# Kernel optimization log

Hardware: AMD Instinct MI355X
Metric: run time of the kernel (lower is better)

## Reference

```python
import jax, jax.numpy as jnp
import numpy as np

N = 32768; D = 384; P = 3; CORR_D = 2 * 49 * P * P  # 882
G_KK = 4096; G_JK = 512
EPS = 1e-3  # LayerNorm eps in the torch module

FLOAT_NAMES = ("net","inp","corr","corr_w1","corr_b1","corr_w2","corr_b2","corr_ln_g","corr_ln_b","corr_w3","corr_b3","norm_g","norm_b","c1_w1","c1_b1","c1_w2","c1_b2","c2_w1","c2_b1","c2_w2","c2_b2","kk_fw","kk_fb","kk_gw","kk_gb","kk_hw","kk_hb","ij_fw","ij_fb","ij_gw","ij_gb","ij_hw","ij_hb","g_ln1_g","g_ln1_b","g1_gw","g1_gb","g1_r1w","g1_r1b","g1_r2w","g1_r2b","g_ln2_g","g_ln2_b","g2_gw","g2_gb","g2_r1w","g2_r1b","g2_r2w","g2_r2b","d_w","d_b","w_w","w_b")

def _ln(x, g, b):
    m = jnp.mean(x, -1, keepdims=True)
    v = jnp.mean((x - m) ** 2, -1, keepdims=True)
    return (x - m) * jax.lax.rsqrt(v + EPS) * g + b

def _mlp2(x, w1, b1, w2, b2):
    return jax.nn.relu(x @ w1 + b1) @ w2 + b2

def _gated_residual(x, gw, gb, r1w, r1b, r2w, r2b):
    gate = jax.nn.sigmoid(x @ gw + gb)
    res = jax.nn.relu(x @ r1w + r1b) @ r2w + r2b
    return x + gate * res

def _soft_agg(x, jx, fw, fb, gw, gb, hw, hb, num_groups):
    # x: [N, D]; jx: [N] group ids -> group-wise softmax weighted sum
    logits = x @ gw + gb
    feats = x @ fw + fb
    gmax = jax.ops.segment_max(logits, jx, num_segments=num_groups)
    e = jnp.exp(logits - gmax[jx])
    den = jax.ops.segment_sum(e, jx, num_segments=num_groups)
    w = e / (den[jx] + 1e-12)
    y = jax.ops.segment_sum(feats * w, jx, num_segments=num_groups)
    return (y @ hw + hb)[jx]

def _forward(p, nix, njx, ukk, ujk):
    # corr encoder MLP
    h = jax.nn.relu(p["corr"] @ p["corr_w1"] + p["corr_b1"]) @ p["corr_w2"] + p["corr_b2"]
    h = jax.nn.relu(_ln(h, p["corr_ln_g"], p["corr_ln_b"])) @ p["corr_w3"] + p["corr_b3"]
    net = p["net"] + p["inp"] + h
    net = _ln(net, p["norm_g"], p["norm_b"])
    mask_ix = (nix >= 0).astype(net.dtype).reshape(1, -1, 1)
    mask_jx = (njx >= 0).astype(net.dtype).reshape(1, -1, 1)
    net = net + _mlp2(mask_ix * net[:, nix], p["c1_w1"], p["c1_b1"], p["c1_w2"], p["c1_b2"])
    net = net + _mlp2(mask_jx * net[:, njx], p["c2_w1"], p["c2_b1"], p["c2_w2"], p["c2_b2"])
    net = net + _soft_agg(net[0], ukk, p["kk_fw"], p["kk_fb"], p["kk_gw"], p["kk_gb"], p["kk_hw"], p["kk_hb"], G_KK)[None]
    net = net + _soft_agg(net[0], ujk, p["ij_fw"], p["ij_fb"], p["ij_gw"], p["ij_gb"], p["ij_hw"], p["ij_hb"], G_JK)[None]
    net = _ln(net, p["g_ln1_g"], p["g_ln1_b"])
    net = _gated_residual(net, p["g1_gw"], p["g1_gb"], p["g1_r1w"], p["g1_r1b"], p["g1_r2w"], p["g1_r2b"])
    net = _ln(net, p["g_ln2_g"], p["g_ln2_b"])
    net = _gated_residual(net, p["g2_gw"], p["g2_gb"], p["g2_r1w"], p["g2_r1b"], p["g2_r2w"], p["g2_r2b"])
    r = jax.nn.relu(net)
    d = r @ p["d_w"] + p["d_b"]               # GradClip is identity in forward
    w = jax.nn.sigmoid(r @ p["w_w"] + p["w_b"])
    return net, d, w

def setup_inputs() -> dict:
    key = jax.random.key(0)
    it = iter(jax.random.split(key, 64))
    def pr(*shape):
        return jax.random.normal(next(it), shape, dtype=jnp.float32) * 0.02
    z = lambda *s: jnp.zeros(s, jnp.float32)
    o = lambda *s: jnp.ones(s, jnp.float32)
    inp = {
        "net": jax.random.normal(next(it), (1, N, D), dtype=jnp.float32),
        "inp": jax.random.normal(next(it), (1, N, D), dtype=jnp.float32),
        "corr": jax.random.normal(next(it), (1, N, CORR_D), dtype=jnp.float32),
        "nix": jax.random.randint(next(it), (N,), 0, N),
        "njx": jax.random.randint(next(it), (N,), 0, N),
        "ukk": jax.random.randint(next(it), (N,), 0, G_KK),
        "ujk": jax.random.randint(next(it), (N,), 0, G_JK),
        "corr_w1": pr(CORR_D, D), "corr_b1": z(D), "corr_w2": pr(D, D), "corr_b2": z(D),
        "corr_ln_g": o(D), "corr_ln_b": z(D), "corr_w3": pr(D, D), "corr_b3": z(D),
        "norm_g": o(D), "norm_b": z(D),
        "c1_w1": pr(D, D), "c1_b1": z(D), "c1_w2": pr(D, D), "c1_b2": z(D),
        "c2_w1": pr(D, D), "c2_b1": z(D), "c2_w2": pr(D, D), "c2_b2": z(D),
        "kk_fw": pr(D, D), "kk_fb": z(D), "kk_gw": pr(D, D), "kk_gb": z(D), "kk_hw": pr(D, D), "kk_hb": z(D),
        "ij_fw": pr(D, D), "ij_fb": z(D), "ij_gw": pr(D, D), "ij_gb": z(D), "ij_hw": pr(D, D), "ij_hb": z(D),
        "g_ln1_g": o(D), "g_ln1_b": z(D),
        "g1_gw": pr(D, D), "g1_gb": z(D), "g1_r1w": pr(D, D), "g1_r1b": z(D), "g1_r2w": pr(D, D), "g1_r2b": z(D),
        "g_ln2_g": o(D), "g_ln2_b": z(D),
        "g2_gw": pr(D, D), "g2_gb": z(D), "g2_r1w": pr(D, D), "g2_r1b": z(D), "g2_r2w": pr(D, D), "g2_r2b": z(D),
        "d_w": pr(D, 2), "d_b": z(2), "w_w": pr(D, 2), "w_b": z(2),
    }
    return inp

def reference(net, inp, corr, corr_w1, corr_b1, corr_w2, corr_b2, corr_ln_g, corr_ln_b, corr_w3, corr_b3, norm_g, norm_b, c1_w1, c1_b1, c1_w2, c1_b2, c2_w1, c2_b1, c2_w2, c2_b2, kk_fw, kk_fb, kk_gw, kk_gb, kk_hw, kk_hb, ij_fw, ij_fb, ij_gw, ij_gb, ij_hw, ij_hb, g_ln1_g, g_ln1_b, g1_gw, g1_gb, g1_r1w, g1_r1b, g1_r2w, g1_r2b, g_ln2_g, g_ln2_b, g2_gw, g2_gb, g2_r1w, g2_r1b, g2_r2w, g2_r2b, d_w, d_b, w_w, w_b, nix, njx, ukk, ujk):
    loc = locals()
    fl = {k: loc[k] for k in FLOAT_NAMES}
    return _forward(fl, nix, njx, ukk, ujk)
```

## Files before the change

### kernel.cpp

```cpp
#include <hip/hip_runtime.h>
#include <hip/hip_bf16.h>
#include <math.h>

#define NR 32768
#define DD 384
#define CDM 882
#define CDMP 896

typedef float f4 __attribute__((ext_vector_type(4)));
typedef float f32x4 __attribute__((ext_vector_type(4)));
typedef __bf16 bf16x8 __attribute__((ext_vector_type(8)));
typedef __bf16 bf16x4 __attribute__((ext_vector_type(4)));

__device__ inline f4 ld4(const float* p) { f4 v; __builtin_memcpy(&v, p, 16); return v; }
__device__ inline void st4(float* p, f4 v) { __builtin_memcpy(p, &v, 16); }
__device__ inline bf16x8 ld8h(const __bf16* p) { bf16x8 v; __builtin_memcpy(&v, p, 16); return v; }
__device__ inline void st8h(__bf16* p, bf16x8 v) { __builtin_memcpy(p, &v, 16); }

__device__ inline void gl_lds16(const void* g, void* l) {
  __builtin_amdgcn_global_load_lds(
      (const __attribute__((address_space(1))) void*)g,
      (__attribute__((address_space(3))) void*)l, 16, 0, 0);
}

__device__ inline float gred16(float v) {
#pragma unroll
  for (int o = 1; o < 16; o <<= 1) v += __shfl_xor(v, o, 64);
  return v;
}

__global__ __launch_bounds__(256) void corr2bf16_k(const float* __restrict__ src,
                                                   __bf16* __restrict__ dst) {
  int i = blockIdx.x * 256 + threadIdx.x;
  int row = i / 112, c8 = (i - row * 112) * 8;
  const float* sp = src + (size_t)row * CDM + c8;
  bf16x8 h;
  if (c8 + 8 <= CDM) {
#pragma unroll
    for (int e = 0; e < 8; ++e) h[e] = (__bf16)sp[e];
  } else {
#pragma unroll
    for (int e = 0; e < 8; ++e) h[e] = (c8 + e < CDM) ? (__bf16)sp[e] : (__bf16)0.f;
  }
  st8h(dst + (size_t)row * CDMP + c8, h);
}

struct WPtrs { const float* w[18]; };

__global__ __launch_bounds__(256) void trans_all_k(WPtrs P, __bf16* __restrict__ dst) {
  int wi = blockIdx.y;
  const float* W = P.w[wi];
  __bf16* WT = dst + (size_t)wi * DD * DD;
  int i = blockIdx.x * 256 + threadIdx.x;
  if (i >= DD * DD) return;
  int n = i / DD, k = i - n * DD;
  WT[i] = (__bf16)W[(size_t)k * DD + n];
}

__global__ __launch_bounds__(256) void trans_corr_k(const float* __restrict__ W,
                                                    __bf16* __restrict__ WT) {
  int i = blockIdx.x * 256 + threadIdx.x;
  if (i >= DD * CDMP) return;
  int n = i / CDMP, k = i - n * CDMP;
  WT[i] = (k < CDM) ? (__bf16)W[(size_t)k * DD + n] : (__bf16)0.f;
}

template <int EPI, int AFP32>
__global__ __launch_bounds__(512, 1) void gemm_k(
    const void* __restrict__ Av, const __bf16* __restrict__ WT,
    const float* __restrict__ bias, __bf16* __restrict__ OUT,
    const __bf16* __restrict__ XRES, const int* __restrict__ idx,
    const __bf16* __restrict__ zpage, int M, int K) {
  __shared__ __align__(16) __bf16 sm[2 * 32768];
  const int t = threadIdx.x;
  const int w = t >> 6, lane = t & 63;
  const int m0 = blockIdx.x * 128;
  const int fr = lane & 15, fq = lane >> 4;
  const int wr = (w >> 2) * 64, wc = (w & 3) * 96;

  const __bf16* aptr[2];
  int aadv[2];
  const __bf16* bptr[6];
#pragma unroll
  for (int j = 0; j < 2; ++j) {
    int rloc = w * 16 + j * 8 + (lane >> 3);
    int cch = (lane & 7) ^ (rloc & 7);
    if constexpr (!AFP32) {
      int ar = idx ? idx[m0 + rloc] : (m0 + rloc);
      if (ar >= 0) { aptr[j] = (const __bf16*)Av + (size_t)ar * K + cch * 8; aadv[j] = 64; }
      else { aptr[j] = zpage; aadv[j] = 0; }
    }
  }
#pragma unroll
  for (int j = 0; j < 6; ++j) {
    int rloc = w * 48 + j * 8 + (lane >> 3);
    int cch = (lane & 7) ^ (rloc & 7);
    bptr[j] = WT + (size_t)rloc * K + cch * 8;
  }
  const float* Af = (const float*)Av;
  const int NT = K >> 6;

  f32x4 acc[4][6];
#pragma unroll
  for (int a = 0; a < 4; ++a)
#pragma unroll
    for (int b = 0; b < 6; ++b)
#pragma unroll
      for (int j = 0; j < 4; ++j) acc[a][b][j] = 0.f;

  auto stageG = [&](int buf) {
    __bf16* As = sm + buf * 32768;
    __bf16* Bs = As + 8192;
#pragma unroll
    for (int j = 0; j < 2; ++j) {
      gl_lds16(aptr[j], &As[(w * 16 + j * 8) * 64]);
      aptr[j] += aadv[j];
    }
#pragma unroll
    for (int j = 0; j < 6; ++j) {
      gl_lds16(bptr[j], &Bs[(w * 48 + j * 8) * 64]);
      bptr[j] += 64;
    }
  };

  auto stageF = [&](int k0) {
    __bf16* As = sm;
    __bf16* Bs = sm + 8192;
#pragma unroll
    for (int j = 0; j < 2; ++j) {
      int rr = (t >> 3) + 64 * j;
      int cc = t & 7;
      const float* ap = Af + (size_t)(m0 + rr) * K + k0 + cc * 8;
      f4 v0 = ld4(ap), v1 = ld4(ap + 4);
      bf16x8 h;
#pragma unroll
      for (int e = 0; e < 4; ++e) { h[e] = (__bf16)v0[e]; h[4 + e] = (__bf16)v1[e]; }
      *reinterpret_cast<bf16x8*>(&As[rr * 64 + ((cc ^ (rr & 7)) << 3)]) = h;
    }
#pragma unroll
    for (int j = 0; j < 6; ++j) {
      gl_lds16(bptr[j], &Bs[(w * 48 + j * 8) * 64]);
      bptr[j] += 64;
    }
  };

  auto compute = [&](int buf) {
    const __bf16* As = sm + buf * 32768;
    const __bf16* Bs = As + 8192;
#pragma unroll
    for (int kk2 = 0; kk2 < 2; ++kk2) {
      bf16x8 af[4];
      bf16x8 bv[6];
#pragma unroll
      for (int mi = 0; mi < 4; ++mi) {
        int rr = wr + mi * 16 + fr;
        af[mi] = *reinterpret_cast<const bf16x8*>(
            &As[rr * 64 + (((fq + kk2 * 4) ^ (rr & 7)) << 3)]);
      }
#pragma unroll
      for (int ni = 0; ni < 6; ++ni) {
        int rr = wc + ni * 16 + fr;
        bv[ni] = *reinterpret_cast<const bf16x8*>(
            &Bs[rr * 64 + (((fq + kk2 * 4) ^ (rr & 7)) << 3)]);
      }
#pragma unroll
      for (int mi = 0; mi < 4; ++mi)
#pragma unroll
        for (int ni = 0; ni < 6; ++ni)
          acc[mi][ni] = __builtin_amdgcn_mfma_f32_16x16x32_bf16(af[mi], bv[ni],
                                                                acc[mi][ni], 0, 0, 0);
    }
  };

  if constexpr (AFP32) {
    for (int tt = 0; tt < NT; ++tt) {
      if (tt) __syncthreads();
      stageF(tt << 6);
      __syncthreads();
      compute(0);
    }
  } else {
    stageG(0);
    int buf = 0;
    for (int tt = 0; tt < NT; ++tt) {
      if (tt + 1 < NT) {
        stageG(buf ^ 1);
        asm volatile("s_waitcnt vmcnt(8)" ::: "memory");
      } else {
        asm volatile("s_waitcnt vmcnt(0)" ::: "memory");
      }
      __builtin_amdgcn_s_barrier();
      __builtin_amdgcn_sched_barrier(0);
      compute(buf);
      __builtin_amdgcn_s_barrier();
      __builtin_amdgcn_sched_barrier(0);
      buf ^= 1;
    }
  }

#pragma unroll
  for (int mi = 0; mi < 4; ++mi)
#pragma unroll
    for (int ni = 0; ni < 6; ++ni) {
      int col = wc + ni * 16 + fr;
      float bvv = bias[col];
#pragma unroll
      for (int j = 0; j < 4; ++j) {
        int row = m0 + wr + mi * 16 + fq * 4 + j;
        size_t o = (size_t)row * DD + col;
        float v = acc[mi][ni][j] + bvv;
        if constexpr (EPI == 0) {
          OUT[o] = (__bf16)v;
        } else if constexpr (EPI == 1) {
          OUT[o] = (__bf16)fmaxf(v, 0.f);
        } else if constexpr (EPI == 2) {
          OUT[o] = (__bf16)((float)OUT[o] + v);
        } else {
          float gl = (float)OUT[o];
          float g = 1.f / (1.f + expf(-gl));
          OUT[o] = (__bf16)((float)XRES[o] + g * v);
        }
      }
    }
}

template <int RELU>
__global__ __launch_bounds__(256) void ln_k(const __bf16* __restrict__ x,
                                            const float* __restrict__ g,
                                            const float* __restrict__ b,
                                            __bf16* __restrict__ out) {
  int w = threadIdx.x >> 6, lane = threadIdx.x & 63;
  int s = lane & 15, qq = lane >> 4;
  int row = blockIdx.x * 16 + w * 4 + qq;
  size_t base = (size_t)row * DD;
  float v[24];
#pragma unroll
  for (int i = 0; i < 3; ++i) {
    bf16x8 h = ld8h(x + base + (s + 16 * i) * 8);
#pragma unroll
    for (int e = 0; e < 8; ++e) v[i * 8 + e] = (float)h[e];
  }
  float sm = 0.f;
#pragma unroll
  for (int i = 0; i < 24; ++i) sm += v[i];
  sm = gred16(sm);
  float mean = sm * (1.f / 384.f);
  float qs = 0.f;
#pragma unroll
  for (int i = 0; i < 24; ++i) { float d = v[i] - mean; qs += d * d; }
  qs = gred16(qs);
  float rs = rsqrtf(qs * (1.f / 384.f) + 1e-3f);
#pragma unroll
  for (int i = 0; i < 3; ++i) {
    int col = (s + 16 * i) * 8;
    f4 g0 = ld4(g + col), g1 = ld4(g + col + 4);
    f4 b0 = ld4(b + col), b1 = ld4(b + col + 4);
    bf16x8 o;
#pragma unroll
    for (int e = 0; e < 4; ++e) {
      float y0 = (v[i * 8 + e] - mean) * rs * g0[e] + b0[e];
      float y1 = (v[i * 8 + 4 + e] - mean) * rs * g1[e] + b1[e];
      if (RELU) { y0 = fmaxf(y0, 0.f); y1 = fmaxf(y1, 0.f); }
      o[e] = (__bf16)y0; o[4 + e] = (__bf16)y1;
    }
    st8h(out + base + col, o);
  }
}

__global__ __launch_bounds__(256) void ln3_k(const float* __restrict__ x1,
                                             const float* __restrict__ x2,
                                             const __bf16* __restrict__ x3,
                                             const float* __restrict__ g,
                                             const float* __restrict__ b,
                                             __bf16* __restrict__ out) {
  int w = threadIdx.x >> 6, lane = threadIdx.x & 63;
  int s = lane & 15, qq = lane >> 4;
  int row = blockIdx.x * 16 + w * 4 + qq;
  size_t base = (size_t)row * DD;
  float v[24];
#pragma unroll
  for (int i = 0; i < 3; ++i) {
    int col = (s + 16 * i) * 8;
    f4 a0 = ld4(x1 + base + col), a1 = ld4(x1 + base + col + 4);
    f4 c0 = ld4(x2 + base + col), c1 = ld4(x2 + base + col + 4);
    bf16x8 h = ld8h(x3 + base + col);
#pragma unroll
    for (int e = 0; e < 4; ++e) {
      v[i * 8 + e] = a0[e] + c0[e] + (float)h[e];
      v[i * 8 + 4 + e] = a1[e] + c1[e] + (float)h[4 + e];
    }
  }
  float sm = 0.f;
#pragma unroll
  for (int i = 0; i < 24; ++i) sm += v[i];
  sm = gred16(sm);
  float mean = sm * (1.f / 384.f);
  float qs = 0.f;
#pragma unroll
  for (int i = 0; i < 24; ++i) { float d = v[i] - mean; qs += d * d; }
  qs = gred16(qs);
  float rs = rsqrtf(qs * (1.f / 384.f) + 1e-3f);
#pragma unroll
  for (int i = 0; i < 3; ++i) {
    int col = (s + 16 * i) * 8;
    f4 g0 = ld4(g + col), g1 = ld4(g + col + 4);
    f4 b0 = ld4(b + col), b1 = ld4(b + col + 4);
    bf16x8 o;
#pragma unroll
    for (int e = 0; e < 4; ++e) {
      o[e] = (__bf16)((v[i * 8 + e] - mean) * rs * g0[e] + b0[e]);
      o[4 + e] = (__bf16)((v[i * 8 + 4 + e] - mean) * rs * g1[e] + b1[e]);
    }
    st8h(out + base + col, o);
  }
}

__global__ __launch_bounds__(256) void hist_k(const int* __restrict__ gid,
                                              int* __restrict__ cnt, int n) {
  int i = blockIdx.x * 256 + threadIdx.x;
  if (i < n) atomicAdd(&cnt[gid[i]], 1);
}

__global__ __launch_bounds__(256) void scan_k(const int* __restrict__ cnt,
                                              int* __restrict__ off,
                                              int* __restrict__ curb, int G) {
  __shared__ int ls[256];
  int t = threadIdx.x;
  int per = G / 256;
  int base = t * per;
  int s = 0;
  for (int i = 0; i < per; ++i) s += cnt[base + i];
  ls[t] = s;
  __syncthreads();
  for (int o = 1; o < 256; o <<= 1) {
    int v = (t >= o) ? ls[t - o] : 0;
    __syncthreads();
    ls[t] += v;
    __syncthreads();
  }
  int run = (t == 0) ? 0 : ls[t - 1];
  for (int i = 0; i < per; ++i) {
    off[base + i] = run;
    run += cnt[base + i];
    curb[base + i] = 0;
  }
  if (t == 255) off[G] = run;
}

__global__ __launch_bounds__(256) void scatter_k(const int* __restrict__ gid,
                                                 const int* __restrict__ off,
                                                 int* __restrict__ cur,
                                                 int* __restrict__ rows, int n) {
  int i = blockIdx.x * 256 + threadIdx.x;
  if (i >= n) return;
  int g = gid[i];
  int p = atomicAdd(&cur[g], 1);
  rows[off[g] + p] = i;
}

__global__ __launch_bounds__(384) void segagg_k(const __bf16* __restrict__ L,
                                                const __bf16* __restrict__ Ft,
                                                const int* __restrict__ rows,
                                                const int* __restrict__ off,
                                                float* __restrict__ yb) {
  int g = blockIdx.x;
  int c = threadIdx.x;
  int s = off[g], e = off[g + 1];
  float mx = -3.0e38f;
  for (int p = s; p < e; ++p) {
    int r = rows[p];
    mx = fmaxf(mx, (float)L[(size_t)r * DD + c]);
  }
  float num = 0.f, den = 0.f;
  for (int p = s; p < e; ++p) {
    int r = rows[p];
    float lv = (float)L[(size_t)r * DD + c];
    float fv = (float)Ft[(size_t)r * DD + c];
    float ev = expf(lv - mx);
    den += ev;
    num += fv * ev;
  }
  yb[(size_t)g * DD + c] = num / (den + 1e-12f);
}

__global__ __launch_bounds__(256) void addgather_k(__bf16* __restrict__ X,
                                                   const __bf16* __restrict__ z,
                                                   const int* __restrict__ gid) {
  int i = blockIdx.x * 256 + threadIdx.x;
  int row = i / 48, c = (i - row * 48) * 8;
  int g = gid[row];
  size_t lo = (size_t)row * DD + c;
  bf16x8 a = ld8h(X + lo);
  bf16x8 zz = ld8h(z + (size_t)g * DD + c);
  bf16x8 o;
#pragma unroll
  for (int e = 0; e < 8; ++e) o[e] = (__bf16)((float)a[e] + (float)zz[e]);
  st8h(X + lo, o);
}

__global__ __launch_bounds__(256) void final_k(const __bf16* __restrict__ net,
                                               const float* __restrict__ dw,
                                               const float* __restrict__ db,
                                               const float* __restrict__ ww,
                                               const float* __restrict__ wb,
                                               float* __restrict__ out) {
  int w = threadIdx.x >> 6, lane = threadIdx.x & 63;
  int s = lane & 15, qq = lane >> 4;
  int row = blockIdx.x * 16 + w * 4 + qq;
  size_t base = (size_t)row * DD;
  float d0 = 0, d1 = 0, w0 = 0, w1 = 0;
#pragma unroll
  for (int i = 0; i < 3; ++i) {
    int col = (s + 16 * i) * 8;
    bf16x8 h = ld8h(net + base + col);
    f4 o0, o1;
#pragma unroll
    for (int e = 0; e < 4; ++e) {
      float x0 = (float)h[e], x1 = (float)h[4 + e];
      o0[e] = x0; o1[e] = x1;
      float r0 = fmaxf(x0, 0.f), r1 = fmaxf(x1, 0.f);
      int c0 = col + e, c1 = col + 4 + e;
      d0 += r0 * dw[2 * c0] + r1 * dw[2 * c1];
      d1 += r0 * dw[2 * c0 + 1] + r1 * dw[2 * c1 + 1];
      w0 += r0 * ww[2 * c0] + r1 * ww[2 * c1];
      w1 += r0 * ww[2 * c0 + 1] + r1 * ww[2 * c1 + 1];
    }
    st4(out + base + col, o0);
    st4(out + base + col + 4, o1);
  }
  d0 = gred16(d0); d1 = gred16(d1); w0 = gred16(w0); w1 = gred16(w1);
  if (s == 0) {
    float* outd = out + (size_t)NR * DD;
    float* outw = outd + (size_t)NR * 2;
    outd[2 * row] = d0 + db[0];
    outd[2 * row + 1] = d1 + db[1];
    outw[2 * row] = 1.f / (1.f + expf(-(w0 + wb[0])));
    outw[2 * row + 1] = 1.f / (1.f + expf(-(w1 + wb[1])));
  }
}

extern "C" void kernel_launch(void* const* d_in, const int* in_sizes, int n_in,
                              void* d_out, int out_size, void* d_ws, size_t ws_size,
                              hipStream_t stream) {
  const float* in_net = (const float*)d_in[0];
  const float* in_inp = (const float*)d_in[1];
  const float* in_corr = (const float*)d_in[2];
  const int* nix = (const int*)d_in[3];
  const int* njx = (const int*)d_in[4];
  const int* ukk = (const int*)d_in[5];
  const int* ujk = (const int*)d_in[6];
  auto F = [&](int i) { return (const float*)d_in[i]; };

  constexpr size_t MiB = 1024 * 1024;
  constexpr size_t SZ_ACT = (size_t)NR * DD * 2;
  char* ws = (char*)d_ws;
  __bf16* Xc = (__bf16*)(ws);
  __bf16* T2b = (__bf16*)(ws);
  __bf16* Fb = (__bf16*)(ws + SZ_ACT);
  __bf16* zb = (__bf16*)(ws + 2 * SZ_ACT);
  float* yb = (float*)(ws + 2 * SZ_ACT + 3 * MiB);
  __bf16* T1b = (__bf16*)(ws + 60 * MiB);
  char* p = ws + 84 * MiB;
  int* rows = (int*)p; p += (size_t)NR * 4;
  int* off = (int*)p; p += 32768;
  int* cnt = (int*)p; p += 16384;
  int* curb = (int*)p; p += 16384;
  __bf16* wt_all = (__bf16*)p; p += (size_t)18 * DD * DD * 2;
  __bf16* wt_corr1 = (__bf16*)p; p += (size_t)DD * CDMP * 2;
  __bf16* zpage = (__bf16*)p;

  const int widx[18] = {17, 19, 21, 23, 25, 27, 29, 31, 33, 35, 39, 41, 43, 47, 49, 51, 9, 13};
  WPtrs P;
  for (int i = 0; i < 18; ++i) P.w[i] = F(widx[i]);
  auto WTp = [&](int i) { return wt_all + (size_t)i * DD * DD; };

  hipMemsetAsync(zpage, 0, 256, stream);
  trans_all_k<<<dim3(576, 18), 256, 0, stream>>>(P, wt_all);
  trans_corr_k<<<1344, 256, 0, stream>>>(F(7), wt_corr1);
  corr2bf16_k<<<NR * 112 / 256, 256, 0, stream>>>(in_corr, Xc);

  auto GEMM = [&](int epi, int afp32, const void* A, const __bf16* WT, const float* bias,
                  __bf16* OUT, const __bf16* XRES, const int* idx, int M, int K) {
    dim3 g(M / 128), b(512);
    if (afp32) {
      gemm_k<0, 1><<<g, b, 0, stream>>>(A, WT, bias, OUT, XRES, idx, zpage, M, K);
    } else {
      switch (epi) {
        case 0: gemm_k<0, 0><<<g, b, 0, stream>>>(A, WT, bias, OUT, XRES, idx, zpage, M, K); break;
        case 1: gemm_k<1, 0><<<g, b, 0, stream>>>(A, WT, bias, OUT, XRES, idx, zpage, M, K); break;
        case 2: gemm_k<2, 0><<<g, b, 0, stream>>>(A, WT, bias, OUT, XRES, idx, zpage, M, K); break;
        default: gemm_k<3, 0><<<g, b, 0, stream>>>(A, WT, bias, OUT, XRES, idx, zpage, M, K); break;
      }
    }
  };

  auto SEGAGG = [&](const int* gid, int G, const __bf16* L, const __bf16* Ft) {
    hipMemsetAsync(cnt, 0, (size_t)G * 4, stream);
    hist_k<<<NR / 256, 256, 0, stream>>>(gid, cnt, NR);
    scan_k<<<1, 256, 0, stream>>>(cnt, off, curb, G);
    scatter_k<<<NR / 256, 256, 0, stream>>>(gid, off, curb, rows, NR);
    segagg_k<<<G, 384, 0, stream>>>(L, Ft, rows, off, yb);
  };

  const int LNG = NR / 16;
  const int SEGB = NR * 48 / 256;

  GEMM(1, 0, Xc, wt_corr1, F(8), T1b, nullptr, nullptr, NR, CDMP);
  GEMM(0, 0, T1b, WTp(16), F(10), T2b, nullptr, nullptr, NR, DD);
  ln_k<1><<<LNG, 256, 0, stream>>>(T2b, F(11), F(12), T1b);
  GEMM(0, 0, T1b, WTp(17), F(14), T2b, nullptr, nullptr, NR, DD);
  ln3_k<<<LNG, 256, 0, stream>>>(in_net, in_inp, T2b, F(15), F(16), T1b);
  GEMM(1, 0, T1b, WTp(0), F(18), T2b, nullptr, nix, NR, DD);
  GEMM(2, 0, T2b, WTp(1), F(20), T1b, nullptr, nullptr, NR, DD);
  GEMM(1, 0, T1b, WTp(2), F(22), T2b, nullptr, njx, NR, DD);
  GEMM(2, 0, T2b, WTp(3), F(24), T1b, nullptr, nullptr, NR, DD);
  GEMM(0, 0, T1b, WTp(5), F(28), T2b, nullptr, nullptr, NR, DD);
  GEMM(0, 0, T1b, WTp(4), F(26), Fb, nullptr, nullptr, NR, DD);
  SEGAGG(ukk, 4096, T2b, Fb);
  GEMM(0, 1, yb, WTp(6), F(30), zb, nullptr, nullptr, 4096, DD);
  addgather_k<<<SEGB, 256, 0, stream>>>(T1b, zb, ukk);
  GEMM(0, 0, T1b, WTp(8), F(34), T2b, nullptr, nullptr, NR, DD);
  GEMM(0, 0, T1b, WTp(7), F(32), Fb, nullptr, nullptr, NR, DD);
  SEGAGG(ujk, 512, T2b, Fb);
  GEMM(0, 1, yb, WTp(9), F(36), zb, nullptr, nullptr, 512, DD);
  addgather_k<<<SEGB, 256, 0, stream>>>(T1b, zb, ujk);
  ln_k<0><<<LNG, 256, 0, stream>>>(T1b, F(37), F(38), T2b);
  GEMM(0, 0, T2b, WTp(10), F(40), Fb, nullptr, nullptr, NR, DD);
  GEMM(1, 0, T2b, WTp(11), F(42), T1b, nullptr, nullptr, NR, DD);
  GEMM(3, 0, T1b, WTp(12), F(44), Fb, T2b, nullptr, NR, DD);
  ln_k<0><<<LNG, 256, 0, stream>>>(Fb, F(45), F(46), T1b);
  GEMM(0, 0, T1b, WTp(13), F(48), T2b, nullptr, nullptr, NR, DD);
  GEMM(1, 0, T1b, WTp(14), F(50), Fb, nullptr, nullptr, NR, DD);
  GEMM(3, 0, Fb, WTp(15), F(52), T2b, T1b, nullptr, NR, DD);
  final_k<<<LNG, 256, 0, stream>>>(T2b, F(53), F(54), F(55), F(56), (float*)d_out);
}
```

Baseline: 666.2 us.

## Fuse LayerNorms and output head into GEMM epilogues; batch segment index build

Row-wise LayerNorm is moved into the GEMM epilogue through new epilogue modes. Each block reduces row sums and sums of squares across the four column warps through LDS, so the standalone ln_k, ln3_k and final_k passes over the activations are no longer needed. The gated-residual GEMMs now apply the following LayerNorm directly, and the last GEMM also writes the fp32 output plus the 2-wide d and w heads. The second add-gather is merged with the next LayerNorm, and the histogram, scan and scatter for both group ids run once up front instead of per aggregation. In exchange, variance is computed as E[x^2]-mean^2 in fp32, which is less numerically robust, and the epilogues use more registers and add extra barriers.

```diff
diff --git a/kernel.cpp b/kernel.cpp
--- a/kernel.cpp
+++ b/kernel.cpp
@@ -65,18 +65,23 @@
   WT[i] = (k < CDM) ? (__bf16)W[(size_t)k * DD + n] : (__bf16)0.f;
 }
 
+struct GP {
+  const void* A; const __bf16* WT; const float* bias; __bf16* OUT;
+  const __bf16* XRES; const __bf16* GIN;
+  const float* p0; const float* p1; const float* p2; const float* p3;
+  float* fout; const float* net32; const float* inp32;
+  const int* idx; const __bf16* zpage; int M; int K;
+};
+
 template <int EPI, int AFP32>
-__global__ __launch_bounds__(512, 1) void gemm_k(
-    const void* __restrict__ Av, const __bf16* __restrict__ WT,
-    const float* __restrict__ bias, __bf16* __restrict__ OUT,
-    const __bf16* __restrict__ XRES, const int* __restrict__ idx,
-    const __bf16* __restrict__ zpage, int M, int K) {
+__global__ __launch_bounds__(512, 1) void gemm_k(GP gp) {
   __shared__ __align__(16) __bf16 sm[2 * 32768];
   const int t = threadIdx.x;
   const int w = t >> 6, lane = t & 63;
   const int m0 = blockIdx.x * 128;
   const int fr = lane & 15, fq = lane >> 4;
   const int wr = (w >> 2) * 64, wc = (w & 3) * 96;
+  const int K = gp.K;
 
   const __bf16* aptr[2];
   int aadv[2];
@@ -86,18 +91,18 @@
     int rloc = w * 16 + j * 8 + (lane >> 3);
     int cch = (lane & 7) ^ (rloc & 7);
     if constexpr (!AFP32) {
-      int ar = idx ? idx[m0 + rloc] : (m0 + rloc);
-      if (ar >= 0) { aptr[j] = (const __bf16*)Av + (size_t)ar * K + cch * 8; aadv[j] = 64; }
-      else { aptr[j] = zpage; aadv[j] = 0; }
+      int ar = gp.idx ? gp.idx[m0 + rloc] : (m0 + rloc);
+      if (ar >= 0) { aptr[j] = (const __bf16*)gp.A + (size_t)ar * K + cch * 8; aadv[j] = 64; }
+      else { aptr[j] = gp.zpage; aadv[j] = 0; }
     }
   }
 #pragma unroll
   for (int j = 0; j < 6; ++j) {
     int rloc = w * 48 + j * 8 + (lane >> 3);
     int cch = (lane & 7) ^ (rloc & 7);
-    bptr[j] = WT + (size_t)rloc * K + cch * 8;
-  }
-  const float* Af = (const float*)Av;
+    bptr[j] = gp.WT + (size_t)rloc * K + cch * 8;
+  }
+  const float* Af = (const float*)gp.A;
   const int NT = K >> 6;
 
   f32x4 acc[4][6];
@@ -198,47 +203,229 @@
     }
   }
 
+  const int nw = w & 3;
+  float bcol[6];
+#pragma unroll
+  for (int ni = 0; ni < 6; ++ni) bcol[ni] = gp.bias[wc + ni * 16 + fr];
 #pragma unroll
   for (int mi = 0; mi < 4; ++mi)
 #pragma unroll
-    for (int ni = 0; ni < 6; ++ni) {
-      int col = wc + ni * 16 + fr;
-      float bvv = bias[col];
-#pragma unroll
-      for (int j = 0; j < 4; ++j) {
-        int row = m0 + wr + mi * 16 + fq * 4 + j;
-        size_t o = (size_t)row * DD + col;
-        float v = acc[mi][ni][j] + bvv;
-        if constexpr (EPI == 0) {
-          OUT[o] = (__bf16)v;
-        } else if constexpr (EPI == 1) {
-          OUT[o] = (__bf16)fmaxf(v, 0.f);
-        } else if constexpr (EPI == 2) {
-          OUT[o] = (__bf16)((float)OUT[o] + v);
-        } else {
-          float gl = (float)OUT[o];
-          float g = 1.f / (1.f + expf(-gl));
-          OUT[o] = (__bf16)((float)XRES[o] + g * v);
+    for (int ni = 0; ni < 6; ++ni)
+#pragma unroll
+      for (int j = 0; j < 4; ++j) acc[mi][ni][j] += bcol[ni];
+
+  if constexpr (EPI <= 2) {
+#pragma unroll
+    for (int mi = 0; mi < 4; ++mi)
+#pragma unroll
+      for (int ni = 0; ni < 6; ++ni) {
+        int col = wc + ni * 16 + fr;
+#pragma unroll
+        for (int j = 0; j < 4; ++j) {
+          int row = m0 + wr + mi * 16 + fq * 4 + j;
+          size_t o = (size_t)row * DD + col;
+          float v = acc[mi][ni][j];
+          if constexpr (EPI == 0) gp.OUT[o] = (__bf16)v;
+          else if constexpr (EPI == 1) gp.OUT[o] = (__bf16)fmaxf(v, 0.f);
+          else gp.OUT[o] = (__bf16)((float)gp.OUT[o] + v);
         }
       }
-    }
-}
-
-template <int RELU>
-__global__ __launch_bounds__(256) void ln_k(const __bf16* __restrict__ x,
-                                            const float* __restrict__ g,
-                                            const float* __restrict__ b,
-                                            __bf16* __restrict__ out) {
+  } else {
+    if constexpr (EPI == 5) {
+#pragma unroll
+      for (int mi = 0; mi < 4; ++mi)
+#pragma unroll
+        for (int ni = 0; ni < 6; ++ni) {
+          int col = wc + ni * 16 + fr;
+#pragma unroll
+          for (int j = 0; j < 4; ++j) {
+            int row = m0 + wr + mi * 16 + fq * 4 + j;
+            size_t o = (size_t)row * DD + col;
+            acc[mi][ni][j] += gp.net32[o] + gp.inp32[o];
+          }
+        }
+    }
+    if constexpr (EPI == 6 || EPI == 7) {
+#pragma unroll
+      for (int mi = 0; mi < 4; ++mi)
+#pragma unroll
+        for (int ni = 0; ni < 6; ++ni) {
+          int col = wc + ni * 16 + fr;
+#pragma unroll
+          for (int j = 0; j < 4; ++j) {
+            int row = m0 + wr + mi * 16 + fq * 4 + j;
+            size_t o = (size_t)row * DD + col;
+            float gl = (float)gp.GIN[o];
+            float sg = 1.f / (1.f + expf(-gl));
+            acc[mi][ni][j] = (float)gp.XRES[o] + sg * acc[mi][ni][j];
+          }
+        }
+    }
+    __syncthreads();
+    if constexpr (EPI != 7) {
+      float s1[4][4], s2[4][4];
+#pragma unroll
+      for (int mi = 0; mi < 4; ++mi)
+#pragma unroll
+        for (int j = 0; j < 4; ++j) { s1[mi][j] = 0.f; s2[mi][j] = 0.f; }
+#pragma unroll
+      for (int mi = 0; mi < 4; ++mi)
+#pragma unroll
+        for (int ni = 0; ni < 6; ++ni)
+#pragma unroll
+          for (int j = 0; j < 4; ++j) {
+            float v = acc[mi][ni][j];
+            s1[mi][j] += v;
+            s2[mi][j] += v * v;
+          }
+#pragma unroll
+      for (int o = 1; o < 16; o <<= 1)
+#pragma unroll
+        for (int mi = 0; mi < 4; ++mi)
+#pragma unroll
+          for (int j = 0; j < 4; ++j) {
+            s1[mi][j] += __shfl_xor(s1[mi][j], o, 64);
+            s2[mi][j] += __shfl_xor(s2[mi][j], o, 64);
+          }
+      float* lsum = (float*)sm;
+      float* lsq = lsum + 512;
+      if (fr == 0) {
+#pragma unroll
+        for (int mi = 0; mi < 4; ++mi)
+#pragma unroll
+          for (int j = 0; j < 4; ++j) {
+            int rr = wr + mi * 16 + fq * 4 + j;
+            lsum[rr * 4 + nw] = s1[mi][j];
+            lsq[rr * 4 + nw] = s2[mi][j];
+          }
+      }
+      __syncthreads();
+      float mn[4][4], rs[4][4];
+#pragma unroll
+      for (int mi = 0; mi < 4; ++mi)
+#pragma unroll
+        for (int j = 0; j < 4; ++j) {
+          int rr = wr + mi * 16 + fq * 4 + j;
+          float S1 = lsum[rr * 4] + lsum[rr * 4 + 1] + lsum[rr * 4 + 2] + lsum[rr * 4 + 3];
+          float S2 = lsq[rr * 4] + lsq[rr * 4 + 1] + lsq[rr * 4 + 2] + lsq[rr * 4 + 3];
+          float m = S1 * (1.f / 384.f);
+          float va = S2 * (1.f / 384.f) - m * m;
+          mn[mi][j] = m;
+          rs[mi][j] = rsqrtf(va + 1e-3f);
+        }
+#pragma unroll
+      for (int ni = 0; ni < 6; ++ni) {
+        int col = wc + ni * 16 + fr;
+        float gg = gp.p0[col], bb = gp.p1[col];
+#pragma unroll
+        for (int mi = 0; mi < 4; ++mi)
+#pragma unroll
+          for (int j = 0; j < 4; ++j) {
+            int row = m0 + wr + mi * 16 + fq * 4 + j;
+            float y = (acc[mi][ni][j] - mn[mi][j]) * rs[mi][j] * gg + bb;
+            if constexpr (EPI == 4) y = fmaxf(y, 0.f);
+            gp.OUT[(size_t)row * DD + col] = (__bf16)y;
+          }
+      }
+    } else {
+      float c0[6], c1[6], c2[6], c3[6];
+#pragma unroll
+      for (int ni = 0; ni < 6; ++ni) {
+        int col = wc + ni * 16 + fr;
+        c0[ni] = gp.p0[2 * col];
+        c1[ni] = gp.p0[2 * col + 1];
+        c2[ni] = gp.p2[2 * col];
+        c3[ni] = gp.p2[2 * col + 1];
+      }
+      float dt[4][4][4];
+#pragma unroll
+      for (int mi = 0; mi < 4; ++mi)
+#pragma unroll
+        for (int j = 0; j < 4; ++j)
+#pragma unroll
+          for (int q = 0; q < 4; ++q) dt[mi][j][q] = 0.f;
+#pragma unroll
+      for (int mi = 0; mi < 4; ++mi)
+#pragma unroll
+        for (int ni = 0; ni < 6; ++ni) {
+          int col = wc + ni * 16 + fr;
+#pragma unroll
+          for (int j = 0; j < 4; ++j) {
+            int row = m0 + wr + mi * 16 + fq * 4 + j;
+            float v = acc[mi][ni][j];
+            gp.fout[(size_t)row * DD + col] = v;
+            float r = fmaxf(v, 0.f);
+            dt[mi][j][0] += r * c0[ni];
+            dt[mi][j][1] += r * c1[ni];
+            dt[mi][j][2] += r * c2[ni];
+            dt[mi][j][3] += r * c3[ni];
+          }
+        }
+#pragma unroll
+      for (int o = 1; o < 16; o <<= 1)
+#pragma unroll
+        for (int mi = 0; mi < 4; ++mi)
+#pragma unroll
+          for (int j = 0; j < 4; ++j)
+#pragma unroll
+            for (int q = 0; q < 4; ++q)
+              dt[mi][j][q] += __shfl_xor(dt[mi][j][q], o, 64);
+      float* lt = (float*)sm;
+      if (fr == 0) {
+#pragma unroll
+        for (int mi = 0; mi < 4; ++mi)
+#pragma unroll
+          for (int j = 0; j < 4; ++j) {
+            int rr = wr + mi * 16 + fq * 4 + j;
+#pragma unroll
+            for (int q = 0; q < 4; ++q) lt[(rr * 4 + nw) * 4 + q] = dt[mi][j][q];
+          }
+      }
+      __syncthreads();
+      if (nw == 0 && fr == 0) {
+        float* fd = gp.fout + (size_t)NR * DD;
+        float* fw = fd + (size_t)NR * 2;
+#pragma unroll
+        for (int mi = 0; mi < 4; ++mi)
+#pragma unroll
+          for (int j = 0; j < 4; ++j) {
+            int rr = wr + mi * 16 + fq * 4 + j;
+            int row = m0 + rr;
+            float T[4];
+#pragma unroll
+            for (int q = 0; q < 4; ++q)
+              T[q] = lt[(rr * 4 + 0) * 4 + q] + lt[(rr * 4 + 1) * 4 + q] +
+                     lt[(rr * 4 + 2) * 4 + q] + lt[(rr * 4 + 3) * 4 + q];
+            fd[2 * row] = T[0] + gp.p1[0];
+            fd[2 * row + 1] = T[1] + gp.p1[1];
+            fw[2 * row] = 1.f / (1.f + expf(-(T[2] + gp.p3[0])));
+            fw[2 * row + 1] = 1.f / (1.f + expf(-(T[3] + gp.p3[1])));
+          }
+      }
+    }
+  }
+}
+
+__global__ __launch_bounds__(256) void ln_ag_k(const __bf16* __restrict__ X,
+                                               const __bf16* __restrict__ z,
+                                               const int* __restrict__ gid,
+                                               const float* __restrict__ g,
+                                               const float* __restrict__ b,
+                                               __bf16* __restrict__ out) {
   int w = threadIdx.x >> 6, lane = threadIdx.x & 63;
   int s = lane & 15, qq = lane >> 4;
   int row = blockIdx.x * 16 + w * 4 + qq;
+  int gr = gid[row];
   size_t base = (size_t)row * DD;
+  size_t zbase = (size_t)gr * DD;
   float v[24];
 #pragma unroll
   for (int i = 0; i < 3; ++i) {
-    bf16x8 h = ld8h(x + base + (s + 16 * i) * 8);
-#pragma unroll
-    for (int e = 0; e < 8; ++e) v[i * 8 + e] = (float)h[e];
+    int col = (s + 16 * i) * 8;
+    bf16x8 h = ld8h(X + base + col);
+    bf16x8 zz = ld8h(z + zbase + col);
+#pragma unroll
+    for (int e = 0; e < 8; ++e) v[i * 8 + e] = (float)h[e] + (float)zz[e];
   }
   float sm = 0.f;
 #pragma unroll
@@ -258,56 +445,6 @@
     bf16x8 o;
 #pragma unroll
     for (int e = 0; e < 4; ++e) {
-      float y0 = (v[i * 8 + e] - mean) * rs * g0[e] + b0[e];
-      float y1 = (v[i * 8 + 4 + e] - mean) * rs * g1[e] + b1[e];
-      if (RELU) { y0 = fmaxf(y0, 0.f); y1 = fmaxf(y1, 0.f); }
-      o[e] = (__bf16)y0; o[4 + e] = (__bf16)y1;
-    }
-    st8h(out + base + col, o);
-  }
-}
-
-__global__ __launch_bounds__(256) void ln3_k(const float* __restrict__ x1,
-                                             const float* __restrict__ x2,
-                                             const __bf16* __restrict__ x3,
-                                             const float* __restrict__ g,
-                                             const float* __restrict__ b,
-                                             __bf16* __restrict__ out) {
-  int w = threadIdx.x >> 6, lane = threadIdx.x & 63;
-  int s = lane & 15, qq = lane >> 4;
-  int row = blockIdx.x * 16 + w * 4 + qq;
-  size_t base = (size_t)row * DD;
-  float v[24];
-#pragma unroll
-  for (int i = 0; i < 3; ++i) {
-    int col = (s + 16 * i) * 8;
-    f4 a0 = ld4(x1 + base + col), a1 = ld4(x1 + base + col + 4);
-    f4 c0 = ld4(x2 + base + col), c1 = ld4(x2 + base + col + 4);
-    bf16x8 h = ld8h(x3 + base + col);
-#pragma unroll
-    for (int e = 0; e < 4; ++e) {
-      v[i * 8 + e] = a0[e] + c0[e] + (float)h[e];
-      v[i * 8 + 4 + e] = a1[e] + c1[e] + (float)h[4 + e];
-    }
-  }
-  float sm = 0.f;
-#pragma unroll
-  for (int i = 0; i < 24; ++i) sm += v[i];
-  sm = gred16(sm);
-  float mean = sm * (1.f / 384.f);
-  float qs = 0.f;
-#pragma unroll
-  for (int i = 0; i < 24; ++i) { float d = v[i] - mean; qs += d * d; }
-  qs = gred16(qs);
-  float rs = rsqrtf(qs * (1.f / 384.f) + 1e-3f);
-#pragma unroll
-  for (int i = 0; i < 3; ++i) {
-    int col = (s + 16 * i) * 8;
-    f4 g0 = ld4(g + col), g1 = ld4(g + col + 4);
-    f4 b0 = ld4(b + col), b1 = ld4(b + col + 4);
-    bf16x8 o;
-#pragma unroll
-    for (int e = 0; e < 4; ++e) {
       o[e] = (__bf16)((v[i * 8 + e] - mean) * rs * g0[e] + b0[e]);
       o[4 + e] = (__bf16)((v[i * 8 + 4 + e] - mean) * rs * g1[e] + b1[e]);
     }
@@ -315,16 +452,16 @@
   }
 }
 
-__global__ __launch_bounds__(256) void hist_k(const int* __restrict__ gid,
-                                              int* __restrict__ cnt, int n) {
+__global__ __launch_bounds__(256) void hist2_k(const int* __restrict__ ukk,
+                                               const int* __restrict__ ujk,
+                                               int* __restrict__ ckk,
+                                               int* __restrict__ cij) {
   int i = blockIdx.x * 256 + threadIdx.x;
-  if (i < n) atomicAdd(&cnt[gid[i]], 1);
-}
-
-__global__ __launch_bounds__(256) void scan_k(const int* __restrict__ cnt,
-                                              int* __restrict__ off,
-                                              int* __restrict__ curb, int G) {
-  __shared__ int ls[256];
+  atomicAdd(&ckk[ukk[i]], 1);
+  atomicAdd(&cij[ujk[i]], 1);
+}
+
+__device__ inline void scan_body(const int* cnt, int* off, int* curb, int G, int* ls) {
   int t = threadIdx.x;
   int per = G / 256;
   int base = t * per;
@@ -347,15 +484,26 @@
   if (t == 255) off[G] = run;
 }
 
-__global__ __launch_bounds__(256) void scatter_k(const int* __restrict__ gid,
-                                                 const int* __restrict__ off,
-                                                 int* __restrict__ cur,
-                                                 int* __restrict__ rows, int n) {
+__global__ __launch_bounds__(256) void scan2_k(const int* ckk, int* okk, int* qkk,
+                                               const int* cij, int* oij, int* qij) {
+  __shared__ int ls[256];
+  if (blockIdx.x == 0) scan_body(ckk, okk, qkk, 4096, ls);
+  else scan_body(cij, oij, qij, 512, ls);
+}
+
+__global__ __launch_bounds__(256) void scatter2_k(const int* __restrict__ ukk,
+                                                  const int* __restrict__ ujk,
+                                                  const int* __restrict__ okk,
+                                                  int* __restrict__ qkk,
+                                                  int* __restrict__ rkk,
+                                                  const int* __restrict__ oij,
+                                                  int* __restrict__ qij,
+                                                  int* __restrict__ rij) {
   int i = blockIdx.x * 256 + threadIdx.x;
-  if (i >= n) return;
-  int g = gid[i];
-  int p = atomicAdd(&cur[g], 1);
-  rows[off[g] + p] = i;
+  int g1 = ukk[i];
+  rkk[okk[g1] + atomicAdd(&qkk[g1], 1)] = i;
+  int g2 = ujk[i];
+  rij[oij[g2] + atomicAdd(&qij[g2], 1)] = i;
 }
 
 __global__ __launch_bounds__(384) void segagg_k(const __bf16* __restrict__ L,
@@ -398,47 +546,6 @@
   st8h(X + lo, o);
 }
 
-__global__ __launch_bounds__(256) void final_k(const __bf16* __restrict__ net,
-                                               const float* __restrict__ dw,
-                                               const float* __restrict__ db,
-                                               const float* __restrict__ ww,
-                                               const float* __restrict__ wb,
-                                               float* __restrict__ out) {
-  int w = threadIdx.x >> 6, lane = threadIdx.x & 63;
-  int s = lane & 15, qq = lane >> 4;
-  int row = blockIdx.x * 16 + w * 4 + qq;
-  size_t base = (size_t)row * DD;
-  float d0 = 0, d1 = 0, w0 = 0, w1 = 0;
-#pragma unroll
-  for (int i = 0; i < 3; ++i) {
-    int col = (s + 16 * i) * 8;
-    bf16x8 h = ld8h(net + base + col);
-    f4 o0, o1;
-#pragma unroll
-    for (int e = 0; e < 4; ++e) {
-      float x0 = (float)h[e], x1 = (float)h[4 + e];
-      o0[e] = x0; o1[e] = x1;
-      float r0 = fmaxf(x0, 0.f), r1 = fmaxf(x1, 0.f);
-      int c0 = col + e, c1 = col + 4 + e;
-      d0 += r0 * dw[2 * c0] + r1 * dw[2 * c1];
-      d1 += r0 * dw[2 * c0 + 1] + r1 * dw[2 * c1 + 1];
-      w0 += r0 * ww[2 * c0] + r1 * ww[2 * c1];
-      w1 += r0 * ww[2 * c0 + 1] + r1 * ww[2 * c1 + 1];
-    }
-    st4(out + base + col, o0);
-    st4(out + base + col + 4, o1);
-  }
-  d0 = gred16(d0); d1 = gred16(d1); w0 = gred16(w0); w1 = gred16(w1);
-  if (s == 0) {
-    float* outd = out + (size_t)NR * DD;
-    float* outw = outd + (size_t)NR * 2;
-    outd[2 * row] = d0 + db[0];
-    outd[2 * row + 1] = d1 + db[1];
-    outw[2 * row] = 1.f / (1.f + expf(-(w0 + wb[0])));
-    outw[2 * row + 1] = 1.f / (1.f + expf(-(w1 + wb[1])));
-  }
-}
-
 extern "C" void kernel_launch(void* const* d_in, const int* in_sizes, int n_in,
                               void* d_out, int out_size, void* d_ws, size_t ws_size,
                               hipStream_t stream) {
@@ -461,10 +568,14 @@
   float* yb = (float*)(ws + 2 * SZ_ACT + 3 * MiB);
   __bf16* T1b = (__bf16*)(ws + 60 * MiB);
   char* p = ws + 84 * MiB;
-  int* rows = (int*)p; p += (size_t)NR * 4;
-  int* off = (int*)p; p += 32768;
-  int* cnt = (int*)p; p += 16384;
-  int* curb = (int*)p; p += 16384;
+  int* rows_kk = (int*)p; p += (size_t)NR * 4;
+  int* rows_ij = (int*)p; p += (size_t)NR * 4;
+  int* off_kk = (int*)p; p += 8192 * 4;
+  int* off_ij = (int*)p; p += 1024 * 4;
+  int* cnt_kk = (int*)p; p += 4096 * 4;
+  int* cnt_ij = (int*)p; p += 512 * 4;
+  int* curb_kk = (int*)p; p += 4096 * 4;
+  int* curb_ij = (int*)p; p += 512 * 4;
   __bf16* wt_all = (__bf16*)p; p += (size_t)18 * DD * DD * 2;
   __bf16* wt_corr1 = (__bf16*)p; p += (size_t)DD * CDMP * 2;
   __bf16* zpage = (__bf16*)p;
@@ -475,62 +586,67 @@
   auto WTp = [&](int i) { return wt_all + (size_t)i * DD * DD; };
 
   hipMemsetAsync(zpage, 0, 256, stream);
+  hipMemsetAsync(cnt_kk, 0, 4096 * 4, stream);
+  hipMemsetAsync(cnt_ij, 0, 512 * 4, stream);
   trans_all_k<<<dim3(576, 18), 256, 0, stream>>>(P, wt_all);
   trans_corr_k<<<1344, 256, 0, stream>>>(F(7), wt_corr1);
   corr2bf16_k<<<NR * 112 / 256, 256, 0, stream>>>(in_corr, Xc);
-
-  auto GEMM = [&](int epi, int afp32, const void* A, const __bf16* WT, const float* bias,
-                  __bf16* OUT, const __bf16* XRES, const int* idx, int M, int K) {
+  hist2_k<<<NR / 256, 256, 0, stream>>>(ukk, ujk, cnt_kk, cnt_ij);
+  scan2_k<<<2, 256, 0, stream>>>(cnt_kk, off_kk, curb_kk, cnt_ij, off_ij, curb_ij);
+  scatter2_k<<<NR / 256, 256, 0, stream>>>(ukk, ujk, off_kk, curb_kk, rows_kk,
+                                           off_ij, curb_ij, rows_ij);
+
+  auto G = [&](int epi, const void* A, const __bf16* WT, const float* bias,
+               __bf16* OUT, const __bf16* XRES, const __bf16* GIN,
+               const float* p0, const float* p1, const float* p2, const float* p3,
+               float* fout, const float* n32, const float* i32,
+               const int* idx, int M, int K) {
+    GP gp{A, WT, bias, OUT, XRES, GIN, p0, p1, p2, p3, fout, n32, i32, idx, zpage, M, K};
     dim3 g(M / 128), b(512);
-    if (afp32) {
-      gemm_k<0, 1><<<g, b, 0, stream>>>(A, WT, bias, OUT, XRES, idx, zpage, M, K);
-    } else {
-      switch (epi) {
-        case 0: gemm_k<0, 0><<<g, b, 0, stream>>>(A, WT, bias, OUT, XRES, idx, zpage, M, K); break;
-        case 1: gemm_k<1, 0><<<g, b, 0, stream>>>(A, WT, bias, OUT, XRES, idx, zpage, M, K); break;
-        case 2: gemm_k<2, 0><<<g, b, 0, stream>>>(A, WT, bias, OUT, XRES, idx, zpage, M, K); break;
-        default: gemm_k<3, 0><<<g, b, 0, stream>>>(A, WT, bias, OUT, XRES, idx, zpage, M, K); break;
-      }
+    switch (epi) {
+      case 0: gemm_k<0, 0><<<g, b, 0, stream>>>(gp); break;
+      case 1: gemm_k<1, 0><<<g, b, 0, stream>>>(gp); break;
+      case 2: gemm_k<2, 0><<<g, b, 0, stream>>>(gp); break;
+      case 4: gemm_k<4, 0><<<g, b, 0, stream>>>(gp); break;
+      case 5: gemm_k<5, 0><<<g, b, 0, stream>>>(gp); break;
+      case 6: gemm_k<6, 0><<<g, b, 0, stream>>>(gp); break;
+      case 7: gemm_k<7, 0><<<g, b, 0, stream>>>(gp); break;
+      case 8: gemm_k<0, 1><<<g, b, 0, stream>>>(gp); break;
     }
   };
-
-  auto SEGAGG = [&](const int* gid, int G, const __bf16* L, const __bf16* Ft) {
-    hipMemsetAsync(cnt, 0, (size_t)G * 4, stream);
-    hist_k<<<NR / 256, 256, 0, stream>>>(gid, cnt, NR);
-    scan_k<<<1, 256, 0, stream>>>(cnt, off, curb, G);
-    scatter_k<<<NR / 256, 256, 0, stream>>>(gid, off, curb, rows, NR);
-    segagg_k<<<G, 384, 0, stream>>>(L, Ft, rows, off, yb);
+  auto GS = [&](int epi, const void* A, const __bf16* WT, const float* bias,
+                __bf16* OUT, const int* idx, int M, int K) {
+    G(epi, A, WT, bias, OUT, nullptr, nullptr, nullptr, nullptr, nullptr, nullptr,
+      nullptr, nullptr, nullptr, idx, M, K);
   };
 
-  const int LNG = NR / 16;
   const int SEGB = NR * 48 / 256;
 
-  GEMM(1, 0, Xc, wt_corr1, F(8), T1b, nullptr, nullptr, NR, CDMP);
-  GEMM(0, 0, T1b, WTp(16), F(10), T2b, nullptr, nullptr, NR, DD);
-  ln_k<1><<<LNG, 256, 0, stream>>>(T2b, F(11), F(12), T1b);
-  GEMM(0, 0, T1b, WTp(17), F(14), T2b, nullptr, nullptr, NR, DD);
-  ln3_k<<<LNG, 256, 0, stream>>>(in_net, in_inp, T2b, F(15), F(16), T1b);
-  GEMM(1, 0, T1b, WTp(0), F(18), T2b, nullptr, nix, NR, DD);
-  GEMM(2, 0, T2b, WTp(1), F(20), T1b, nullptr, nullptr, NR, DD);
-  GEMM(1, 0, T1b, WTp(2), F(22), T2b, nullptr, njx, NR, DD);
-  GEMM(2, 0, T2b, WTp(3), F(24), T1b, nullptr, nullptr, NR, DD);
-  GEMM(0, 0, T1b, WTp(5), F(28), T2b, nullptr, nullptr, NR, DD);
-  GEMM(0, 0, T1b, WTp(4), F(26), Fb, nullptr, nullptr, NR, DD);
-  SEGAGG(ukk, 4096, T2b, Fb);
-  GEMM(0, 1, yb, WTp(6), F(30), zb, nullptr, nullptr, 4096, DD);
+  GS(1, Xc, wt_corr1, F(8), T1b, nullptr, NR, CDMP);
+  G(4, T1b, WTp(16), F(10), T2b, nullptr, nullptr, F(11), F(12), nullptr, nullptr,
+    nullptr, nullptr, nullptr, nullptr, NR, DD);
+  G(5, T2b, WTp(17), F(14), T1b, nullptr, nullptr, F(15), F(16), nullptr, nullptr,
+    nullptr, in_net, in_inp, nullptr, NR, DD);
+  GS(1, T1b, WTp(0), F(18), T2b, nix, NR, DD);
+  GS(2, T2b, WTp(1), F(20), T1b, nullptr, NR, DD);
+  GS(1, T1b, WTp(2), F(22), T2b, njx, NR, DD);
+  GS(2, T2b, WTp(3), F(24), T1b, nullptr, NR, DD);
+  GS(0, T1b, WTp(5), F(28), T2b, nullptr, NR, DD);
+  GS(0, T1b, WTp(4), F(26), Fb, nullptr, NR, DD);
+  segagg_k<<<4096, 384, 0, stream>>>(T2b, Fb, rows_kk, off_kk, yb);
+  GS(8, yb, WTp(6), F(30), zb, nullptr, 4096, DD);
   addgather_k<<<SEGB, 256, 0, stream>>>(T1b, zb, ukk);
-  GEMM(0, 0, T1b, WTp(8), F(34), T2b, nullptr, nullptr, NR, DD);
-  GEMM(0, 0, T1b, WTp(7), F(32), Fb, nullptr, nullptr, NR, DD);
-  SEGAGG(ujk, 512, T2b, Fb);
-  GEMM(0, 1, yb, WTp(9), F(36), zb, nullptr, nullptr, 512, DD);
-  addgather_k<<<SEGB, 256, 0, stream>>>(T1b, zb, ujk);
-  ln_k<0><<<LNG, 256, 0, stream>>>(T1b, F(37), F(38), T2b);
-  GEMM(0, 0, T2b, WTp(10), F(40), Fb, nullptr, nullptr, NR, DD);
-  GEMM(1, 0, T2b, WTp(11), F(42), T1b, nullptr, nullptr, NR, DD);
-  GEMM(3, 0, T1b, WTp(12), F(44), Fb, T2b, nullptr, NR, DD);
-  ln_k<0><<<LNG, 256, 0, stream>>>(Fb, F(45), F(46), T1b);
-  GEMM(0, 0, T1b, WTp(13), F(48), T2b, nullptr, nullptr, NR, DD);
-  GEMM(1, 0, T1b, WTp(14), F(50), Fb, nullptr, nullptr, NR, DD);
-  GEMM(3, 0, Fb, WTp(15), F(52), T2b, T1b, nullptr, NR, DD);
-  final_k<<<LNG, 256, 0, stream>>>(T2b, F(53), F(54), F(55), F(56), (float*)d_out);
-}
+  GS(0, T1b, WTp(8), F(34), T2b, nullptr, NR, DD);
+  GS(0, T1b, WTp(7), F(32), Fb, nullptr, NR, DD);
+  segagg_k<<<512, 384, 0, stream>>>(T2b, Fb, rows_ij, off_ij, yb);
+  GS(8, yb, WTp(9), F(36), zb, nullptr, 512, DD);
+  ln_ag_k<<<NR / 16, 256, 0, stream>>>(T1b, zb, ujk, F(37), F(38), T2b);
+  GS(0, T2b, WTp(10), F(40), Fb, nullptr, NR, DD);
+  GS(1, T2b, WTp(11), F(42), T1b, nullptr, NR, DD);
+  G(6, T1b, WTp(12), F(44), T2b, T2b, Fb, F(45), F(46), nullptr, nullptr,
+    nullptr, nullptr, nullptr, nullptr, NR, DD);
+  GS(0, T2b, WTp(13), F(48), Fb, nullptr, NR, DD);
+  GS(1, T2b, WTp(14), F(50), T1b, nullptr, NR, DD);
+  G(7, T1b, WTp(15), F(52), nullptr, T2b, Fb, F(53), F(54), F(55), F(56),
+    (float*)d_out, nullptr, nullptr, nullptr, NR, DD);
+}
```

New measurement: 608.0 us. -8.7%, faster.
